# Performance work log

Measured on AMD Instinct MI355X. Metric: run time of the kernel, lower is better.

Reference implementation:

```python
import jax, jax.numpy as jnp
import numpy as np

T_IN, B, H = 24, 8192, 512
T_OUT, OVERLAP, PE_DIM = 12, 4, 4

def setup_inputs() -> dict:
    key = jax.random.key(0)
    ks = jax.random.split(key, 10)
    s = 1.0 / np.sqrt(H)
    return {
        "encoder_out": jax.random.normal(ks[0], (T_IN, B, H), jnp.float32),
        "encoder_hid": jax.random.normal(ks[1], (B, H), jnp.float32),
        "last": jax.random.normal(ks[2], (B, OVERLAP), jnp.float32),
        "pos_embed": jax.random.normal(ks[3], (T_OUT, PE_DIM), jnp.float32),
        "W_ih": jax.random.uniform(ks[4], (3 * H, OVERLAP + PE_DIM), jnp.float32, -s, s),
        "W_hh": jax.random.uniform(ks[5], (3 * H, H), jnp.float32, -s, s),
        "b_ih": jax.random.uniform(ks[6], (3 * H,), jnp.float32, -s, s),
        "b_hh": jax.random.uniform(ks[7], (3 * H,), jnp.float32, -s, s),
        "W_lin": jax.random.uniform(ks[8], (1, 2 * H), jnp.float32, -s, s),
        "b_lin": jax.random.uniform(ks[9], (1,), jnp.float32, -s, s),
    }

def reference(encoder_out, encoder_hid, last, pos_embed, W_ih, W_hh, b_ih, b_hh, W_lin, b_lin):
    batch = encoder_hid.shape[0]
    n_out = pos_embed.shape[0]
    overlap = last.shape[1]

    def gru_cell(x, h):
        gi = x @ W_ih.T + b_ih          # (B, 3H)
        gh = h @ W_hh.T + b_hh          # (B, 3H)
        i_r, i_z, i_n = jnp.split(gi, 3, axis=-1)
        h_r, h_z, h_n = jnp.split(gh, 3, axis=-1)
        r = jax.nn.sigmoid(i_r + h_r)
        z = jax.nn.sigmoid(i_z + h_z)
        n = jnp.tanh(i_n + r * h_n)
        return (1.0 - z) * n + z * h

    def step_fn(carry, step):
        hidden, last_in = carry
        # Bahdanau-style additive attention over encoder timesteps
        attn = jnp.einsum('tbh,bh->tb', encoder_out, hidden)
        attn = jax.nn.softmax(attn, axis=0)
        context = jnp.einsum('tbh,tb->bh', encoder_out, attn)  # (B, H)
        hidden = hidden + context
        pe = jnp.broadcast_to(pos_embed[step], (batch, pos_embed.shape[1]))
        decode_last = jnp.concatenate([last_in, pe], axis=-1)  # (B, overlap+4)
        hidden = gru_cell(decode_last, hidden)
        out = jnp.concatenate([hidden, context], axis=-1) @ W_lin.T + b_lin  # (B, 1)
        new_last = jnp.concatenate(
            [jax.lax.stop_gradient(out), last_in[:, : overlap - 1]], axis=-1)
        return (hidden, new_last), out[:, 0]

    (_, _), outs = jax.lax.scan(step_fn, (encoder_hid, last), jnp.arange(n_out))
    return outs.T  # (B, num_timesteps_output)
```

## Files before the change

### kernel.cpp

```cpp
#include <hip/hip_runtime.h>

#define T_IN   24
#define NB     8192
#define HD     512
#define T_OUT  12

typedef float  f32x4  __attribute__((ext_vector_type(4)));
typedef short  bf16x8 __attribute__((ext_vector_type(8)));

#define GLD16(g, l) __builtin_amdgcn_global_load_lds( \
    (__attribute__((address_space(1))) void*)(g), \
    (__attribute__((address_space(3))) void*)(l), 16, 0, 0)

__device__ __forceinline__ unsigned short f2bf(float f){
  unsigned u = __float_as_uint(f);
  u += 0x7fffu + ((u >> 16) & 1u);
  return (unsigned short)(u >> 16);
}
__device__ __forceinline__ float bf2f(unsigned short h){
  return __uint_as_float(((unsigned)h) << 16);
}
__device__ __forceinline__ float wsum(float v){
  #pragma unroll
  for (int o = 32; o; o >>= 1) v += __shfl_xor(v, o);
  return v;
}

__global__ __launch_bounds__(256) void conv_whh(const float* __restrict__ W,
                                                unsigned short* __restrict__ hi,
                                                unsigned short* __restrict__ lo){
  int idx = blockIdx.x * 256 + threadIdx.x;
  int j = idx >> 9, k = idx & 511;
  float v = W[idx];
  unsigned short h = f2bf(v);
  int o = ((k >> 5) * 1536 + j) * 32 + (k & 31);
  hi[o] = h;
  lo[o] = f2bf(v - bf2f(h));
}

__global__ __launch_bounds__(256, 4) void attn_step(
    const float* __restrict__ enc,
    const float* __restrict__ hid_in,
    const float* __restrict__ Wlin,
    const float* __restrict__ blin,
    const float* __restrict__ last_init,
    float* __restrict__ last_ws,
    float* __restrict__ ctxdot,
    unsigned short* __restrict__ h2hi,
    unsigned short* __restrict__ h2lo,
    float* __restrict__ outp,
    int step, int rev)
{
  __shared__ float lpart[4][28];
  __shared__ float po_s[4];
  __shared__ float red2[4];
  __shared__ float wts_s[T_IN];

  const int b   = rev ? (NB - 1 - (int)blockIdx.x) : (int)blockIdx.x;
  const int tid = threadIdx.x;
  const int l   = tid & 63;
  const int w   = tid >> 6;
  const int c0  = 2 * tid;

  float2 e[T_IN];
  #pragma unroll
  for (int t = 0; t < T_IN; t++)
    e[t] = *(const float2*)(enc + ((size_t)t * NB + b) * HD + c0);
  float2 hh  = *(const float2*)(hid_in + (size_t)b * HD + c0);
  float2 wl0 = *(const float2*)(Wlin + c0);
  float2 wl1 = *(const float2*)(Wlin + HD + c0);

  float p[T_IN];
  #pragma unroll
  for (int t = 0; t < T_IN; t++) p[t] = e[t].x * hh.x + e[t].y * hh.y;

  float po = hh.x * wl0.x + hh.y * wl0.y;
  po = wsum(po);
  if (l == 0) po_s[w] = po;

  const int b0 = l & 1, b1 = (l >> 1) & 1, b2 = (l >> 2) & 1;
  float q[12];
  #pragma unroll
  for (int j = 0; j < 12; j++){
    float send = b0 ? p[j] : p[12 + j];
    float keep = b0 ? p[12 + j] : p[j];
    q[j] = keep + __shfl_xor(send, 1);
  }
  float r6[6];
  #pragma unroll
  for (int j = 0; j < 6; j++){
    float send = b1 ? q[j] : q[6 + j];
    float keep = b1 ? q[6 + j] : q[j];
    r6[j] = keep + __shfl_xor(send, 2);
  }
  float s3[3];
  #pragma unroll
  for (int j = 0; j < 3; j++){
    float send = b2 ? r6[j] : r6[3 + j];
    float keep = b2 ? r6[3 + j] : r6[j];
    s3[j] = keep + __shfl_xor(send, 4);
  }
  #pragma unroll
  for (int j = 0; j < 3; j++){
    s3[j] += __shfl_xor(s3[j], 8);
    s3[j] += __shfl_xor(s3[j], 16);
    s3[j] += __shfl_xor(s3[j], 32);
  }
  if (l < 8){
    int tb = 12 * b0 + 6 * b1 + 3 * b2;
    lpart[w][tb + 0] = s3[0];
    lpart[w][tb + 1] = s3[1];
    lpart[w][tb + 2] = s3[2];
  }
  __syncthreads();

  if (w == 0){
    float v = -3.0e38f;
    if (l < T_IN) v = lpart[0][l] + lpart[1][l] + lpart[2][l] + lpart[3][l];
    float m = v;
    #pragma unroll
    for (int o = 32; o; o >>= 1) m = fmaxf(m, __shfl_xor(m, o));
    float ex = (l < T_IN) ? exp2f((v - m) * 1.44269504f) : 0.f;
    float s = wsum(ex);
    if (l < T_IN) wts_s[l] = ex / s;
  }
  if (w == 1 && l == 0){
    if (step > 0){
      float val = po_s[0] + po_s[1] + po_s[2] + po_s[3] + ctxdot[b];
      outp[(size_t)b * T_OUT + (step - 1)] = val;
      float4 old = *(const float4*)(last_ws + (size_t)b * 4);
      float4 nl; nl.x = val; nl.y = old.x; nl.z = old.y; nl.w = old.z;
      *(float4*)(last_ws + (size_t)b * 4) = nl;
    } else {
      *(float4*)(last_ws + (size_t)b * 4) = *(const float4*)(last_init + (size_t)b * 4);
    }
  }
  __syncthreads();

  float c0v = 0.f, c1v = 0.f;
  #pragma unroll
  for (int t = 0; t < T_IN; t++){
    float wt = wts_s[t];
    c0v += wt * e[t].x;
    c1v += wt * e[t].y;
  }
  float h20 = hh.x + c0v;
  float h21 = hh.y + c1v;
  size_t base = (size_t)b * HD + c0;
  unsigned short q0 = f2bf(h20), q1 = f2bf(h21);
  *(unsigned int*)(h2hi + base) = (unsigned)q0 | ((unsigned)q1 << 16);
  unsigned short r0 = f2bf(h20 - bf2f(q0)), r1 = f2bf(h21 - bf2f(q1));
  *(unsigned int*)(h2lo + base) = (unsigned)r0 | ((unsigned)r1 << 16);

  float pc = c0v * wl1.x + c1v * wl1.y;
  pc = wsum(pc);
  if (l == 0) red2[w] = pc;
  __syncthreads();
  if (tid == 0) ctxdot[b] = red2[0] + red2[1] + red2[2] + red2[3] + blin[0];
}

__global__ __launch_bounds__(512, 4) void gru_gemm(
    const unsigned short* __restrict__ Ahi,
    const unsigned short* __restrict__ Alo,
    const unsigned short* __restrict__ Bhi,
    const unsigned short* __restrict__ Blo,
    const float* __restrict__ last_ws,
    const float* __restrict__ pe,
    const float* __restrict__ W_ih,
    const float* __restrict__ b_ih,
    const float* __restrict__ b_hh,
    float* __restrict__ hidden,
    int step)
{
  __shared__ __align__(16) unsigned short smem[2 * 8192];
  const int tid = threadIdx.x;
  const int bid = blockIdx.x;
  const int xk  = bid & 7;
  const int sl  = bid >> 3;
  const int xt  = (xk << 3) | (sl >> 3);
  const int yt  = sl & 7;
  const int b0  = xt * 128;
  const int n0  = yt * 64;
  const int l   = tid & 63;
  const int wv  = tid >> 6;
  const int wm  = wv >> 2;
  const int wn  = wv & 3;
  const int lr  = l & 15;
  const int lkb = (l >> 4) << 4;

  f32x4 acc[3][4];
  #pragma unroll
  for (int g = 0; g < 3; g++)
    #pragma unroll
    for (int mi = 0; mi < 4; mi++)
      acc[g][mi] = (f32x4){0.f, 0.f, 0.f, 0.f};

  auto stageA = [&](int kt, int buf){
    unsigned short* sb = smem + buf * 8192;
    int row = tid >> 2;
    int pb  = (tid & 3) << 4;
    int ke  = (pb ^ ((row & 3) << 4)) >> 1;
    size_t ga = (size_t)(b0 + row) * HD + kt * 32 + ke;
    GLD16(Ahi + ga, sb + tid * 8);
    GLD16(Alo + ga, sb + 4096 + tid * 8);
  };

  stageA(0, 0);
  for (int kt = 0; kt < 16; kt++){
    const int cur = kt & 1;
    __syncthreads();
    if (kt + 1 < 16) stageA(kt + 1, cur ^ 1);
    const unsigned short* sb = smem + cur * 8192;
    bf16x8 ah[4], al[4];
    #pragma unroll
    for (int mi = 0; mi < 4; mi++){
      int row = wm * 64 + mi * 16 + lr;
      int o = row * 32 + ((lkb ^ ((row & 3) << 4)) >> 1);
      ah[mi] = *(const bf16x8*)(sb + o);
      al[mi] = *(const bf16x8*)(sb + 4096 + o);
    }
    #pragma unroll
    for (int g = 0; g < 3; g++){
      size_t boff = ((size_t)kt * 1536 + g * 512 + n0 + wn * 16 + lr) * 32 + ((l >> 4) << 3);
      bf16x8 bh = *(const bf16x8*)(Bhi + boff);
      bf16x8 bl = *(const bf16x8*)(Blo + boff);
      #pragma unroll
      for (int mi = 0; mi < 4; mi++){
        acc[g][mi] = __builtin_amdgcn_mfma_f32_16x16x32_bf16(ah[mi], bh, acc[g][mi], 0, 0, 0);
        acc[g][mi] = __builtin_amdgcn_mfma_f32_16x16x32_bf16(al[mi], bh, acc[g][mi], 0, 0, 0);
        acc[g][mi] = __builtin_amdgcn_mfma_f32_16x16x32_bf16(ah[mi], bl, acc[g][mi], 0, 0, 0);
      }
    }
  }

  const float pe0 = pe[step * 4 + 0], pe1 = pe[step * 4 + 1],
              pe2 = pe[step * 4 + 2], pe3 = pe[step * 4 + 3];
  const int jg = n0 + wn * 16 + lr;
  const float* wrp = W_ih + (size_t)jg * 8;
  const float* wzp = W_ih + (size_t)(512 + jg) * 8;
  const float* wnp = W_ih + (size_t)(1024 + jg) * 8;
  float4 wr0 = *(const float4*)wrp, wr1 = *(const float4*)(wrp + 4);
  float4 wz0 = *(const float4*)wzp, wz1 = *(const float4*)(wzp + 4);
  float4 wn0 = *(const float4*)wnp, wn1 = *(const float4*)(wnp + 4);
  float cr = pe0*wr1.x + pe1*wr1.y + pe2*wr1.z + pe3*wr1.w + b_ih[jg]       + b_hh[jg];
  float cz = pe0*wz1.x + pe1*wz1.y + pe2*wz1.z + pe3*wz1.w + b_ih[512+jg]   + b_hh[512+jg];
  float cn = pe0*wn1.x + pe1*wn1.y + pe2*wn1.z + pe3*wn1.w + b_ih[1024+jg];
  const float bhn = b_hh[1024 + jg];

  #pragma unroll
  for (int mi = 0; mi < 4; mi++){
    #pragma unroll
    for (int q = 0; q < 4; q++){
      int brow = wm * 64 + mi * 16 + ((l >> 4) << 2) + q;
      size_t bg = (size_t)(b0 + brow);
      float4 x = *(const float4*)(last_ws + bg * 4);
      float gr = x.x*wr0.x + x.y*wr0.y + x.z*wr0.z + x.w*wr0.w + cr + acc[0][mi][q];
      float gz = x.x*wz0.x + x.y*wz0.y + x.z*wz0.z + x.w*wz0.w + cz + acc[1][mi][q];
      float gn = x.x*wn0.x + x.y*wn0.y + x.z*wn0.z + x.w*wn0.w + cn;
      float r = 1.f / (1.f + exp2f(-1.44269504f * gr));
      float z = 1.f / (1.f + exp2f(-1.44269504f * gz));
      float nn = gn + r * (acc[2][mi][q] + bhn);
      float th = 1.f - 2.f / (1.f + exp2f(2.88539008f * nn));
      size_t hoff = bg * HD + jg;
      float h = bf2f(Ahi[hoff]) + bf2f(Alo[hoff]);
      hidden[hoff] = (1.f - z) * th + z * h;
    }
  }
}

__global__ __launch_bounds__(256) void final_out(
    const float* __restrict__ hidden, const float* __restrict__ Wlin,
    const float* __restrict__ ctxdot, float* __restrict__ outp)
{
  int tid = threadIdx.x; int l = tid & 63; int w = tid >> 6;
  int b = blockIdx.x * 4 + w;
  const float* hb = hidden + (size_t)b * HD;
  float p = 0.f;
  #pragma unroll
  for (int j = 0; j < 8; j++) p += hb[l + 64 * j] * Wlin[l + 64 * j];
  p = wsum(p);
  if (l == 0) outp[(size_t)b * T_OUT + 11] = p + ctxdot[b];
}

extern "C" void kernel_launch(void* const* d_in, const int* in_sizes, int n_in,
                              void* d_out, int out_size, void* d_ws, size_t ws_size,
                              hipStream_t stream){
  (void)in_sizes; (void)n_in; (void)out_size; (void)ws_size;
  const float* enc   = (const float*)d_in[0];
  const float* ehid  = (const float*)d_in[1];
  const float* last0 = (const float*)d_in[2];
  const float* pe    = (const float*)d_in[3];
  const float* W_ih  = (const float*)d_in[4];
  const float* W_hh  = (const float*)d_in[5];
  const float* b_ih  = (const float*)d_in[6];
  const float* b_hh  = (const float*)d_in[7];
  const float* W_lin = (const float*)d_in[8];
  const float* b_lin = (const float*)d_in[9];
  float* outp = (float*)d_out;

  char* ws = (char*)d_ws;
  size_t off = 0;
  auto alloc = [&](size_t bytes){ void* p = ws + off; off += (bytes + 255) & ~(size_t)255; return p; };
  unsigned short* whh_hi = (unsigned short*)alloc((size_t)1536 * 512 * 2);
  unsigned short* whh_lo = (unsigned short*)alloc((size_t)1536 * 512 * 2);
  unsigned short* h2hi   = (unsigned short*)alloc((size_t)NB * HD * 2);
  unsigned short* h2lo   = (unsigned short*)alloc((size_t)NB * HD * 2);
  float*          hidden = (float*)         alloc((size_t)NB * HD * 4);
  float*          lastw  = (float*)         alloc((size_t)NB * 4 * 4);
  float*          ctxd   = (float*)         alloc((size_t)NB * 4);

  conv_whh<<<3072, 256, 0, stream>>>(W_hh, whh_hi, whh_lo);
  for (int s = 0; s < T_OUT; s++){
    attn_step<<<NB, 256, 0, stream>>>(enc, s == 0 ? ehid : hidden, W_lin, b_lin,
                                      last0, lastw, ctxd, h2hi, h2lo, outp, s, s & 1);
    gru_gemm<<<512, 512, 0, stream>>>(h2hi, h2lo, whh_hi, whh_lo,
                                      lastw, pe, W_ih, b_ih, b_hh, hidden, s);
  }
  final_out<<<2048, 256, 0, stream>>>(hidden, W_lin, ctxd, outp);
}
```

Before: 1.463 ms.

## Fuse attention and GRU GEMM into one kernel, pipelining batch halves

Merges the attention and GRU GEMM kernels into a single launch whose blocks are either GEMM tiles or attention blocks. The batch is split into two halves so the GEMM for one half runs concurrently with the attention for the other half, in a staggered schedule across steps. Each attention block now processes two batch rows with 512 threads. The goal is to overlap memory-bound attention with MFMA-bound GEMM and to cut idle tails between dependent launches. In exchange, shared memory is sized for the GEMM even in attention blocks, which can lower occupancy, and the half-batch GEMM grid has fewer blocks.

```diff
diff --git a/kernel.cpp b/kernel.cpp
--- a/kernel.cpp
+++ b/kernel.cpp
@@ -4,6 +4,7 @@
 #define NB     8192
 #define HD     512
 #define T_OUT  12
+#define HB     4096
 
 typedef float  f32x4  __attribute__((ext_vector_type(4)));
 typedef short  bf16x8 __attribute__((ext_vector_type(8)));
@@ -19,11 +20,6 @@
 }
 __device__ __forceinline__ float bf2f(unsigned short h){
   return __uint_as_float(((unsigned)h) << 16);
-}
-__device__ __forceinline__ float wsum(float v){
-  #pragma unroll
-  for (int o = 32; o; o >>= 1) v += __shfl_xor(v, o);
-  return v;
 }
 
 __global__ __launch_bounds__(256) void conv_whh(const float* __restrict__ W,
@@ -38,9 +34,9 @@
   lo[o] = f2bf(v - bf2f(h));
 }
 
-__global__ __launch_bounds__(256, 4) void attn_step(
+__global__ __launch_bounds__(512, 4) void fused(
     const float* __restrict__ enc,
-    const float* __restrict__ hid_in,
+    const float* __restrict__ hid_attn,
     const float* __restrict__ Wlin,
     const float* __restrict__ blin,
     const float* __restrict__ last_init,
@@ -48,25 +44,135 @@
     float* __restrict__ ctxdot,
     unsigned short* __restrict__ h2hi,
     unsigned short* __restrict__ h2lo,
+    const unsigned short* __restrict__ Bhi,
+    const unsigned short* __restrict__ Blo,
+    const float* __restrict__ pe,
+    const float* __restrict__ W_ih,
+    const float* __restrict__ b_ih,
+    const float* __restrict__ b_hh,
+    float* __restrict__ hidden,
     float* __restrict__ outp,
-    int step, int rev)
+    int ngemm, int gemm_base, int gstep,
+    int attn_base, int astep, int rev)
 {
-  __shared__ float lpart[4][28];
-  __shared__ float po_s[4];
-  __shared__ float red2[4];
-  __shared__ float wts_s[T_IN];
-
-  const int b   = rev ? (NB - 1 - (int)blockIdx.x) : (int)blockIdx.x;
+  __shared__ __align__(16) unsigned short smem[2 * 8192];
+  __shared__ float lpart[2][4][28];
+  __shared__ float po_s[2][4];
+  __shared__ float red2[2][4];
+  __shared__ float wts_s[2][28];
+
   const int tid = threadIdx.x;
-  const int l   = tid & 63;
-  const int w   = tid >> 6;
-  const int c0  = 2 * tid;
+
+  if ((int)blockIdx.x < ngemm){
+    const int bid = blockIdx.x;
+    const int xk  = bid & 7;
+    const int sl  = bid >> 3;
+    const int xt  = (xk << 2) | (sl >> 3);
+    const int yt  = sl & 7;
+    const int b0  = gemm_base + xt * 128;
+    const int n0  = yt * 64;
+    const int l   = tid & 63;
+    const int wv  = tid >> 6;
+    const int wm  = wv >> 2;
+    const int wn  = wv & 3;
+    const int lr  = l & 15;
+    const int lkb = (l >> 4) << 4;
+
+    f32x4 acc[3][4];
+    #pragma unroll
+    for (int g = 0; g < 3; g++)
+      #pragma unroll
+      for (int mi = 0; mi < 4; mi++)
+        acc[g][mi] = (f32x4){0.f, 0.f, 0.f, 0.f};
+
+    auto stageA = [&](int kt, int buf){
+      unsigned short* sb = smem + buf * 8192;
+      int row = tid >> 2;
+      int pb  = (tid & 3) << 4;
+      int ke  = (pb ^ ((row & 3) << 4)) >> 1;
+      size_t ga = (size_t)(b0 + row) * HD + kt * 32 + ke;
+      GLD16(h2hi + ga, sb + tid * 8);
+      GLD16(h2lo + ga, sb + 4096 + tid * 8);
+    };
+
+    stageA(0, 0);
+    for (int kt = 0; kt < 16; kt++){
+      const int cur = kt & 1;
+      __syncthreads();
+      if (kt + 1 < 16) stageA(kt + 1, cur ^ 1);
+      const unsigned short* sb = smem + cur * 8192;
+      bf16x8 ah[4], al[4];
+      #pragma unroll
+      for (int mi = 0; mi < 4; mi++){
+        int row = wm * 64 + mi * 16 + lr;
+        int o = row * 32 + ((lkb ^ ((row & 3) << 4)) >> 1);
+        ah[mi] = *(const bf16x8*)(sb + o);
+        al[mi] = *(const bf16x8*)(sb + 4096 + o);
+      }
+      #pragma unroll
+      for (int g = 0; g < 3; g++){
+        size_t boff = ((size_t)kt * 1536 + g * 512 + n0 + wn * 16 + lr) * 32 + ((l >> 4) << 3);
+        bf16x8 bh = *(const bf16x8*)(Bhi + boff);
+        bf16x8 bl = *(const bf16x8*)(Blo + boff);
+        #pragma unroll
+        for (int mi = 0; mi < 4; mi++){
+          acc[g][mi] = __builtin_amdgcn_mfma_f32_16x16x32_bf16(ah[mi], bh, acc[g][mi], 0, 0, 0);
+          acc[g][mi] = __builtin_amdgcn_mfma_f32_16x16x32_bf16(al[mi], bh, acc[g][mi], 0, 0, 0);
+          acc[g][mi] = __builtin_amdgcn_mfma_f32_16x16x32_bf16(ah[mi], bl, acc[g][mi], 0, 0, 0);
+        }
+      }
+    }
+
+    const float pe0 = pe[gstep * 4 + 0], pe1 = pe[gstep * 4 + 1],
+                pe2 = pe[gstep * 4 + 2], pe3 = pe[gstep * 4 + 3];
+    const int jg = n0 + wn * 16 + lr;
+    const float* wrp = W_ih + (size_t)jg * 8;
+    const float* wzp = W_ih + (size_t)(512 + jg) * 8;
+    const float* wnp = W_ih + (size_t)(1024 + jg) * 8;
+    float4 wr0 = *(const float4*)wrp, wr1 = *(const float4*)(wrp + 4);
+    float4 wz0 = *(const float4*)wzp, wz1 = *(const float4*)(wzp + 4);
+    float4 wn0 = *(const float4*)wnp, wn1 = *(const float4*)(wnp + 4);
+    float cr = pe0*wr1.x + pe1*wr1.y + pe2*wr1.z + pe3*wr1.w + b_ih[jg]       + b_hh[jg];
+    float cz = pe0*wz1.x + pe1*wz1.y + pe2*wz1.z + pe3*wz1.w + b_ih[512+jg]   + b_hh[512+jg];
+    float cn = pe0*wn1.x + pe1*wn1.y + pe2*wn1.z + pe3*wn1.w + b_ih[1024+jg];
+    const float bhn = b_hh[1024 + jg];
+
+    #pragma unroll
+    for (int mi = 0; mi < 4; mi++){
+      #pragma unroll
+      for (int q = 0; q < 4; q++){
+        int brow = wm * 64 + mi * 16 + ((l >> 4) << 2) + q;
+        size_t bg = (size_t)(b0 + brow);
+        float4 x = *(const float4*)(last_ws + bg * 4);
+        float gr = x.x*wr0.x + x.y*wr0.y + x.z*wr0.z + x.w*wr0.w + cr + acc[0][mi][q];
+        float gz = x.x*wz0.x + x.y*wz0.y + x.z*wz0.z + x.w*wz0.w + cz + acc[1][mi][q];
+        float gn = x.x*wn0.x + x.y*wn0.y + x.z*wn0.z + x.w*wn0.w + cn;
+        float r = 1.f / (1.f + exp2f(-1.44269504f * gr));
+        float z = 1.f / (1.f + exp2f(-1.44269504f * gz));
+        float nn = gn + r * (acc[2][mi][q] + bhn);
+        float th = 1.f - 2.f / (1.f + exp2f(2.88539008f * nn));
+        size_t hoff = bg * HD + jg;
+        float h = bf2f(h2hi[hoff]) + bf2f(h2lo[hoff]);
+        hidden[hoff] = (1.f - z) * th + z * h;
+      }
+    }
+    return;
+  }
+
+  const int bpi  = (int)blockIdx.x - ngemm;
+  const int half = tid >> 8;
+  const int stid = tid & 255;
+  const int l    = stid & 63;
+  const int w    = stid >> 6;
+  const int bp   = rev ? (HB / 2 - 1 - bpi) : bpi;
+  const int b    = attn_base + bp * 2 + half;
+  const int c0   = 2 * stid;
 
   float2 e[T_IN];
   #pragma unroll
   for (int t = 0; t < T_IN; t++)
     e[t] = *(const float2*)(enc + ((size_t)t * NB + b) * HD + c0);
-  float2 hh  = *(const float2*)(hid_in + (size_t)b * HD + c0);
+  float2 hh  = *(const float2*)(hid_attn + (size_t)b * HD + c0);
   float2 wl0 = *(const float2*)(Wlin + c0);
   float2 wl1 = *(const float2*)(Wlin + HD + c0);
 
@@ -75,29 +181,30 @@
   for (int t = 0; t < T_IN; t++) p[t] = e[t].x * hh.x + e[t].y * hh.y;
 
   float po = hh.x * wl0.x + hh.y * wl0.y;
-  po = wsum(po);
-  if (l == 0) po_s[w] = po;
-
-  const int b0 = l & 1, b1 = (l >> 1) & 1, b2 = (l >> 2) & 1;
-  float q[12];
+  #pragma unroll
+  for (int o = 32; o; o >>= 1) po += __shfl_xor(po, o);
+  if (l == 0) po_s[half][w] = po;
+
+  const int b0_ = l & 1, b1_ = (l >> 1) & 1, b2_ = (l >> 2) & 1;
+  float q12[12];
   #pragma unroll
   for (int j = 0; j < 12; j++){
-    float send = b0 ? p[j] : p[12 + j];
-    float keep = b0 ? p[12 + j] : p[j];
-    q[j] = keep + __shfl_xor(send, 1);
+    float send = b0_ ? p[j] : p[12 + j];
+    float keep = b0_ ? p[12 + j] : p[j];
+    q12[j] = keep + __shfl_xor(send, 1);
   }
   float r6[6];
   #pragma unroll
   for (int j = 0; j < 6; j++){
-    float send = b1 ? q[j] : q[6 + j];
-    float keep = b1 ? q[6 + j] : q[j];
+    float send = b1_ ? q12[j] : q12[6 + j];
+    float keep = b1_ ? q12[6 + j] : q12[j];
     r6[j] = keep + __shfl_xor(send, 2);
   }
   float s3[3];
   #pragma unroll
   for (int j = 0; j < 3; j++){
-    float send = b2 ? r6[j] : r6[3 + j];
-    float keep = b2 ? r6[3 + j] : r6[j];
+    float send = b2_ ? r6[j] : r6[3 + j];
+    float keep = b2_ ? r6[3 + j] : r6[j];
     s3[j] = keep + __shfl_xor(send, 4);
   }
   #pragma unroll
@@ -107,27 +214,30 @@
     s3[j] += __shfl_xor(s3[j], 32);
   }
   if (l < 8){
-    int tb = 12 * b0 + 6 * b1 + 3 * b2;
-    lpart[w][tb + 0] = s3[0];
-    lpart[w][tb + 1] = s3[1];
-    lpart[w][tb + 2] = s3[2];
+    int tb = 12 * b0_ + 6 * b1_ + 3 * b2_;
+    lpart[half][w][tb + 0] = s3[0];
+    lpart[half][w][tb + 1] = s3[1];
+    lpart[half][w][tb + 2] = s3[2];
   }
   __syncthreads();
 
   if (w == 0){
     float v = -3.0e38f;
-    if (l < T_IN) v = lpart[0][l] + lpart[1][l] + lpart[2][l] + lpart[3][l];
+    if (l < T_IN)
+      v = lpart[half][0][l] + lpart[half][1][l] + lpart[half][2][l] + lpart[half][3][l];
     float m = v;
     #pragma unroll
     for (int o = 32; o; o >>= 1) m = fmaxf(m, __shfl_xor(m, o));
     float ex = (l < T_IN) ? exp2f((v - m) * 1.44269504f) : 0.f;
-    float s = wsum(ex);
-    if (l < T_IN) wts_s[l] = ex / s;
+    float s = ex;
+    #pragma unroll
+    for (int o = 32; o; o >>= 1) s += __shfl_xor(s, o);
+    if (l < T_IN) wts_s[half][l] = ex / s;
   }
   if (w == 1 && l == 0){
-    if (step > 0){
-      float val = po_s[0] + po_s[1] + po_s[2] + po_s[3] + ctxdot[b];
-      outp[(size_t)b * T_OUT + (step - 1)] = val;
+    if (astep > 0){
+      float val = po_s[half][0] + po_s[half][1] + po_s[half][2] + po_s[half][3] + ctxdot[b];
+      outp[(size_t)b * T_OUT + (astep - 1)] = val;
       float4 old = *(const float4*)(last_ws + (size_t)b * 4);
       float4 nl; nl.x = val; nl.y = old.x; nl.z = old.y; nl.w = old.z;
       *(float4*)(last_ws + (size_t)b * 4) = nl;
@@ -140,7 +250,7 @@
   float c0v = 0.f, c1v = 0.f;
   #pragma unroll
   for (int t = 0; t < T_IN; t++){
-    float wt = wts_s[t];
+    float wt = wts_s[half][t];
     c0v += wt * e[t].x;
     c1v += wt * e[t].y;
   }
@@ -153,119 +263,12 @@
   *(unsigned int*)(h2lo + base) = (unsigned)r0 | ((unsigned)r1 << 16);
 
   float pc = c0v * wl1.x + c1v * wl1.y;
-  pc = wsum(pc);
-  if (l == 0) red2[w] = pc;
+  #pragma unroll
+  for (int o = 32; o; o >>= 1) pc += __shfl_xor(pc, o);
+  if (l == 0) red2[half][w] = pc;
   __syncthreads();
-  if (tid == 0) ctxdot[b] = red2[0] + red2[1] + red2[2] + red2[3] + blin[0];
-}
-
-__global__ __launch_bounds__(512, 4) void gru_gemm(
-    const unsigned short* __restrict__ Ahi,
-    const unsigned short* __restrict__ Alo,
-    const unsigned short* __restrict__ Bhi,
-    const unsigned short* __restrict__ Blo,
-    const float* __restrict__ last_ws,
-    const float* __restrict__ pe,
-    const float* __restrict__ W_ih,
-    const float* __restrict__ b_ih,
-    const float* __restrict__ b_hh,
-    float* __restrict__ hidden,
-    int step)
-{
-  __shared__ __align__(16) unsigned short smem[2 * 8192];
-  const int tid = threadIdx.x;
-  const int bid = blockIdx.x;
-  const int xk  = bid & 7;
-  const int sl  = bid >> 3;
-  const int xt  = (xk << 3) | (sl >> 3);
-  const int yt  = sl & 7;
-  const int b0  = xt * 128;
-  const int n0  = yt * 64;
-  const int l   = tid & 63;
-  const int wv  = tid >> 6;
-  const int wm  = wv >> 2;
-  const int wn  = wv & 3;
-  const int lr  = l & 15;
-  const int lkb = (l >> 4) << 4;
-
-  f32x4 acc[3][4];
-  #pragma unroll
-  for (int g = 0; g < 3; g++)
-    #pragma unroll
-    for (int mi = 0; mi < 4; mi++)
-      acc[g][mi] = (f32x4){0.f, 0.f, 0.f, 0.f};
-
-  auto stageA = [&](int kt, int buf){
-    unsigned short* sb = smem + buf * 8192;
-    int row = tid >> 2;
-    int pb  = (tid & 3) << 4;
-    int ke  = (pb ^ ((row & 3) << 4)) >> 1;
-    size_t ga = (size_t)(b0 + row) * HD + kt * 32 + ke;
-    GLD16(Ahi + ga, sb + tid * 8);
-    GLD16(Alo + ga, sb + 4096 + tid * 8);
-  };
-
-  stageA(0, 0);
-  for (int kt = 0; kt < 16; kt++){
-    const int cur = kt & 1;
-    __syncthreads();
-    if (kt + 1 < 16) stageA(kt + 1, cur ^ 1);
-    const unsigned short* sb = smem + cur * 8192;
-    bf16x8 ah[4], al[4];
-    #pragma unroll
-    for (int mi = 0; mi < 4; mi++){
-      int row = wm * 64 + mi * 16 + lr;
-      int o = row * 32 + ((lkb ^ ((row & 3) << 4)) >> 1);
-      ah[mi] = *(const bf16x8*)(sb + o);
-      al[mi] = *(const bf16x8*)(sb + 4096 + o);
-    }
-    #pragma unroll
-    for (int g = 0; g < 3; g++){
-      size_t boff = ((size_t)kt * 1536 + g * 512 + n0 + wn * 16 + lr) * 32 + ((l >> 4) << 3);
-      bf16x8 bh = *(const bf16x8*)(Bhi + boff);
-      bf16x8 bl = *(const bf16x8*)(Blo + boff);
-      #pragma unroll
-      for (int mi = 0; mi < 4; mi++){
-        acc[g][mi] = __builtin_amdgcn_mfma_f32_16x16x32_bf16(ah[mi], bh, acc[g][mi], 0, 0, 0);
-        acc[g][mi] = __builtin_amdgcn_mfma_f32_16x16x32_bf16(al[mi], bh, acc[g][mi], 0, 0, 0);
-        acc[g][mi] = __builtin_amdgcn_mfma_f32_16x16x32_bf16(ah[mi], bl, acc[g][mi], 0, 0, 0);
-      }
-    }
-  }
-
-  const float pe0 = pe[step * 4 + 0], pe1 = pe[step * 4 + 1],
-              pe2 = pe[step * 4 + 2], pe3 = pe[step * 4 + 3];
-  const int jg = n0 + wn * 16 + lr;
-  const float* wrp = W_ih + (size_t)jg * 8;
-  const float* wzp = W_ih + (size_t)(512 + jg) * 8;
-  const float* wnp = W_ih + (size_t)(1024 + jg) * 8;
-  float4 wr0 = *(const float4*)wrp, wr1 = *(const float4*)(wrp + 4);
-  float4 wz0 = *(const float4*)wzp, wz1 = *(const float4*)(wzp + 4);
-  float4 wn0 = *(const float4*)wnp, wn1 = *(const float4*)(wnp + 4);
-  float cr = pe0*wr1.x + pe1*wr1.y + pe2*wr1.z + pe3*wr1.w + b_ih[jg]       + b_hh[jg];
-  float cz = pe0*wz1.x + pe1*wz1.y + pe2*wz1.z + pe3*wz1.w + b_ih[512+jg]   + b_hh[512+jg];
-  float cn = pe0*wn1.x + pe1*wn1.y + pe2*wn1.z + pe3*wn1.w + b_ih[1024+jg];
-  const float bhn = b_hh[1024 + jg];
-
-  #pragma unroll
-  for (int mi = 0; mi < 4; mi++){
-    #pragma unroll
-    for (int q = 0; q < 4; q++){
-      int brow = wm * 64 + mi * 16 + ((l >> 4) << 2) + q;
-      size_t bg = (size_t)(b0 + brow);
-      float4 x = *(const float4*)(last_ws + bg * 4);
-      float gr = x.x*wr0.x + x.y*wr0.y + x.z*wr0.z + x.w*wr0.w + cr + acc[0][mi][q];
-      float gz = x.x*wz0.x + x.y*wz0.y + x.z*wz0.z + x.w*wz0.w + cz + acc[1][mi][q];
-      float gn = x.x*wn0.x + x.y*wn0.y + x.z*wn0.z + x.w*wn0.w + cn;
-      float r = 1.f / (1.f + exp2f(-1.44269504f * gr));
-      float z = 1.f / (1.f + exp2f(-1.44269504f * gz));
-      float nn = gn + r * (acc[2][mi][q] + bhn);
-      float th = 1.f - 2.f / (1.f + exp2f(2.88539008f * nn));
-      size_t hoff = bg * HD + jg;
-      float h = bf2f(Ahi[hoff]) + bf2f(Alo[hoff]);
-      hidden[hoff] = (1.f - z) * th + z * h;
-    }
-  }
+  if (stid == 0)
+    ctxdot[b] = red2[half][0] + red2[half][1] + red2[half][2] + red2[half][3] + blin[0];
 }
 
 __global__ __launch_bounds__(256) void final_out(
@@ -278,7 +281,8 @@
   float p = 0.f;
   #pragma unroll
   for (int j = 0; j < 8; j++) p += hb[l + 64 * j] * Wlin[l + 64 * j];
-  p = wsum(p);
+  #pragma unroll
+  for (int o = 32; o; o >>= 1) p += __shfl_xor(p, o);
   if (l == 0) outp[(size_t)b * T_OUT + 11] = p + ctxdot[b];
 }
 
@@ -310,11 +314,24 @@
   float*          ctxd   = (float*)         alloc((size_t)NB * 4);
 
   conv_whh<<<3072, 256, 0, stream>>>(W_hh, whh_hi, whh_lo);
-  for (int s = 0; s < T_OUT; s++){
-    attn_step<<<NB, 256, 0, stream>>>(enc, s == 0 ? ehid : hidden, W_lin, b_lin,
-                                      last0, lastw, ctxd, h2hi, h2lo, outp, s, s & 1);
-    gru_gemm<<<512, 512, 0, stream>>>(h2hi, h2lo, whh_hi, whh_lo,
-                                      lastw, pe, W_ih, b_ih, b_hh, hidden, s);
+
+  fused<<<2048, 512, 0, stream>>>(enc, ehid, W_lin, b_lin, last0, lastw, ctxd,
+                                  h2hi, h2lo, whh_hi, whh_lo, pe, W_ih, b_ih, b_hh,
+                                  hidden, outp, 0, 0, 0,  0, 0, 0);
+  for (int k = 0; k < T_OUT; k++){
+    fused<<<256 + 2048, 512, 0, stream>>>(enc, k == 0 ? ehid : hidden, W_lin, b_lin,
+                                          last0, lastw, ctxd, h2hi, h2lo,
+                                          whh_hi, whh_lo, pe, W_ih, b_ih, b_hh,
+                                          hidden, outp,
+                                          256,  0, k,
+                                           HB, k, k & 1);
+    int nblk = (k < T_OUT - 1) ? (256 + 2048) : 256;
+    fused<<<nblk, 512, 0, stream>>>(enc, hidden, W_lin, b_lin,
+                                    last0, lastw, ctxd, h2hi, h2lo,
+                                    whh_hi, whh_lo, pe, W_ih, b_ih, b_hh,
+                                    hidden, outp,
+                                    256,  HB, k,
+                                     0, k + 1, (k + 1) & 1);
   }
   final_out<<<2048, 256, 0, stream>>>(hidden, W_lin, ctxd, outp);
 }
```

Result: slower. 1.615 ms (+10.4%).
